# Performance work log

Hardware: AMD Instinct MI355X
Metric: run time of the kernel (lower is better)

Reference implementation:

```python
import jax, jax.numpy as jnp
import numpy as np

N = 50000; E = 120000; FN = 64; EA = 16; R = 4; H = 4; HID = 128; L = 3
NIDS = 10001; IDE = 32; RED = 8; NG = 64; NC = 10; KH = 128; GRID = 5; ORD = 3
EDIM = EA + RED; FFH = 256; GK = GRID + ORD


def layernorm(x, w, b):
    m = x.mean(-1, keepdims=True)
    v = ((x - m) ** 2).mean(-1, keepdims=True)
    return (x - m) / jnp.sqrt(v + 1e-5) * w + b


def b_splines(x, grid, k):
    # x: (B, in); grid: (in, G + 2k + 1) -> bases: (B, in, G + k)
    xe = x[..., None]
    bases = ((xe >= grid[:, :-1]) & (xe < grid[:, 1:])).astype(x.dtype)
    for j in range(1, k + 1):
        bases = ((xe - grid[:, :-(j + 1)]) / (grid[:, j:-1] - grid[:, :-(j + 1)]) * bases[..., :-1]
                 + (grid[:, j + 1:] - xe) / (grid[:, j + 1:] - grid[:, 1:-j]) * bases[..., 1:])
    return bases


def kan_linear(x, bw, sw, sc, grid):
    base = jax.nn.silu(x) @ bw.T
    B = b_splines(x, grid, ORD)
    return base + jnp.einsum('big,oig->bo', B, sw * sc[..., None])


def make_grid(in_features):
    h = 2.0 / GRID
    g = np.arange(-ORD, GRID + ORD + 1) * h - 1.0
    return jnp.asarray(np.tile(g, (in_features, 1)), dtype=jnp.float32)


def setup_inputs():
    key = jax.random.key(0)
    ks = jax.random.split(key, 24)
    s = 0.02
    inp = {}
    inp['x'] = jax.random.normal(ks[0], (N, FN), jnp.float32)
    inp['edge_attr'] = jax.random.normal(ks[1], (E, EA), jnp.float32)
    inp['id_token'] = jax.random.randint(ks[2], (N,), 0, NIDS)
    inp['edge_index'] = jax.random.randint(ks[3], (2, E), 0, N)
    inp['edge_type'] = jax.random.randint(ks[4], (E,), 0, R)
    inp['batch'] = jnp.sort(jax.random.randint(ks[5], (N,), 0, NG))
    inp['id_emb_table'] = jax.random.normal(ks[6], (NIDS, IDE)) * s
    inp['in_proj_w'] = jax.random.normal(ks[7], (HID, FN + IDE)) * s
    inp['in_proj_b'] = jnp.zeros((HID,))
    inp['rel_emb'] = jax.random.normal(ks[8], (L, R, RED)) * s
    inp['lin_l_w'] = jax.random.normal(ks[9], (L, R, H * HID, HID)) * s
    inp['lin_l_b'] = jnp.zeros((L, R, H * HID))
    inp['lin_r_w'] = jax.random.normal(ks[10], (L, R, H * HID, HID)) * s
    inp['lin_r_b'] = jnp.zeros((L, R, H * HID))
    inp['lin_edge_w'] = jax.random.normal(ks[11], (L, R, H * HID, EDIM)) * s
    inp['att_w'] = jax.random.normal(ks[12], (L, R, H, HID)) * s
    inp['conv_bias'] = jnp.zeros((L, R, HID))
    inp['rel_gate'] = jnp.zeros((L, R))
    inp['norm1_w'] = jnp.ones((L, HID)); inp['norm1_b'] = jnp.zeros((L, HID))
    inp['norm2_w'] = jnp.ones((L, HID)); inp['norm2_b'] = jnp.zeros((L, HID))
    inp['ffn_w1'] = jax.random.normal(ks[13], (L, FFH, HID)) * s
    inp['ffn_b1'] = jnp.zeros((L, FFH))
    inp['ffn_w2'] = jax.random.normal(ks[14], (L, HID, FFH)) * s
    inp['ffn_b2'] = jnp.zeros((L, HID))
    inp['readout_norm_w'] = jnp.ones((2 * HID,)); inp['readout_norm_b'] = jnp.zeros((2 * HID,))
    inp['base_w1'] = jax.random.normal(ks[15], (KH, 2 * HID)) * s
    inp['spline_w1'] = jax.random.normal(ks[16], (KH, 2 * HID, GK)) * s
    inp['spline_scaler1'] = jnp.ones((KH, 2 * HID))
    inp['grid1'] = make_grid(2 * HID)
    inp['base_w2'] = jax.random.normal(ks[17], (NC, KH)) * s
    inp['spline_w2'] = jax.random.normal(ks[18], (NC, KH, GK)) * s
    inp['spline_scaler2'] = jnp.ones((NC, KH))
    inp['grid2'] = make_grid(KH)
    return inp


def reference(x, edge_attr, id_token, edge_index, edge_type, batch,
              id_emb_table, in_proj_w, in_proj_b, rel_emb,
              lin_l_w, lin_l_b, lin_r_w, lin_r_b, lin_edge_w, att_w, conv_bias,
              rel_gate, norm1_w, norm1_b, norm2_w, norm2_b,
              ffn_w1, ffn_b1, ffn_w2, ffn_b2, readout_norm_w, readout_norm_b,
              base_w1, spline_w1, spline_scaler1, grid1,
              base_w2, spline_w2, spline_scaler2, grid2):
    src, dst = edge_index[0], edge_index[1]
    h = jnp.concatenate([x, id_emb_table[id_token]], -1)
    h = jax.nn.silu(h @ in_proj_w.T + in_proj_b)  # input_proj (eval: no dropout)
    for l in range(L):
        gate = jax.nn.softmax(rel_gate[l])  # all relations present w.h.p.
        h_msg = jnp.zeros_like(h)
        for r in range(R):
            maskf = (edge_type == r).astype(h.dtype)
            ea = jnp.concatenate([edge_attr, jnp.broadcast_to(rel_emb[l, r], (E, RED))], -1)
            xl = (h @ lin_l_w[l, r].T + lin_l_b[l, r]).reshape(N, H, HID)
            xr = (h @ lin_r_w[l, r].T + lin_r_b[l, r]).reshape(N, H, HID)
            ee = (ea @ lin_edge_w[l, r].T).reshape(E, H, HID)
            sfeat = jax.nn.leaky_relu(xl[src] + xr[dst] + ee, negative_slope=0.2)
            logit = jnp.einsum('ehc,hc->eh', sfeat, att_w[l, r])
            logit = jnp.where(maskf[:, None] > 0, logit, -1e9)
            m = jax.ops.segment_max(logit, dst, num_segments=N)
            a = jnp.exp(logit - m[dst]) * maskf[:, None]
            den = jax.ops.segment_sum(a, dst, num_segments=N)
            a = a / jnp.where(den == 0, 1.0, den)[dst]
            out = jax.ops.segment_sum(a[:, :, None] * xl[src], dst, num_segments=N)
            out = out.mean(1) + conv_bias[l, r]  # concat=False -> head mean
            h_msg = h_msg + gate[r] * out
        h = layernorm(h + h_msg, norm1_w[l], norm1_b[l])
        f = jax.nn.silu(h @ ffn_w1[l].T + ffn_b1[l]) @ ffn_w2[l].T + ffn_b2[l]
        h = layernorm(h + f, norm2_w[l], norm2_b[l])
    cnt = jax.ops.segment_sum(jnp.ones((N,), h.dtype), batch, num_segments=NG)
    hmean = jax.ops.segment_sum(h, batch, num_segments=NG) / jnp.maximum(cnt, 1.0)[:, None]
    hmax = jax.ops.segment_max(h, batch, num_segments=NG)
    g = layernorm(jnp.concatenate([hmean, hmax], -1), readout_norm_w, readout_norm_b)
    z = kan_linear(g, base_w1, spline_w1, spline_scaler1, grid1)
    logits = kan_linear(z, base_w2, spline_w2, spline_scaler2, grid2)
    return logits
```

## Files before the change

kernel.cpp:

```cpp
#include <hip/hip_runtime.h>
#include <math.h>

#define NN 50000
#define NE 120000
#define FN 64
#define NEA 16
#define NR 4
#define NH 4
#define HID 128
#define NL 3
#define IDE 32
#define RED 8
#define NG 64
#define NC 10
#define KH 128
#define FFH 256
#define NBIN (NR * NN)
#define SCAN_BLK ((NBIN + 1023) / 1024)
#define CAPS 32768
#define CAPH 9216

typedef short bf16x8 __attribute__((ext_vector_type(8)));
typedef float f32x4 __attribute__((ext_vector_type(4)));

__device__ __forceinline__ unsigned short f2b(float f) {
  unsigned u = __float_as_uint(f);
  unsigned r = (u + 0x7FFFu + ((u >> 16) & 1u)) >> 16;
  return (unsigned short)r;
}
__device__ __forceinline__ float b2f(unsigned short b) {
  return __uint_as_float((unsigned)b << 16);
}

__global__ void cvt_bf16(const float* __restrict__ s, unsigned short* __restrict__ d, int n4) {
  int i = blockIdx.x * blockDim.x + threadIdx.x;
  if (i >= n4) return;
  float4 v = ((const float4*)s)[i];
  ushort4 o;
  o.x = f2b(v.x); o.y = f2b(v.y); o.z = f2b(v.z); o.w = f2b(v.w);
  ((ushort4*)d)[i] = o;
}

template <int KT>
__device__ __forceinline__ void gemm_direct(
    const unsigned short* __restrict__ A, const int* __restrict__ rowlist,
    const unsigned short* __restrict__ W, const float* __restrict__ bias,
    float* __restrict__ Cf, unsigned short* __restrict__ Cb,
    int nrows, int mout, int act, int rowBase, int colBase) {
  constexpr int NK = KT / 32;
  __shared__ unsigned short Es[64][136];
  int t = threadIdx.x;
  int lane = t & 63, w = t >> 6;
  int wm = w >> 1, wn = w & 1;
  int q = lane >> 4, mr = lane & 15;

  const unsigned short* ap[2];
#pragma unroll
  for (int mt = 0; mt < 2; ++mt) {
    int gr = rowBase + wm * 32 + mt * 16 + mr;
    int cg = (gr < nrows) ? gr : 0;
    int ar = rowlist ? rowlist[cg] : cg;
    ap[mt] = A + (size_t)ar * KT + q * 8;
  }
  const unsigned short* wp[4];
#pragma unroll
  for (int nt = 0; nt < 4; ++nt)
    wp[nt] = W + (size_t)(colBase + wn * 64 + nt * 16 + mr) * KT + q * 8;

  f32x4 acc[2][4] = {};
#pragma unroll
  for (int k = 0; k < NK; ++k) {
    bf16x8 af[2], bfr[4];
#pragma unroll
    for (int mt = 0; mt < 2; ++mt) af[mt] = *(const bf16x8*)(ap[mt] + k * 32);
#pragma unroll
    for (int nt = 0; nt < 4; ++nt) bfr[nt] = *(const bf16x8*)(wp[nt] + k * 32);
#pragma unroll
    for (int mt = 0; mt < 2; ++mt)
#pragma unroll
      for (int nt = 0; nt < 4; ++nt)
        acc[mt][nt] = __builtin_amdgcn_mfma_f32_16x16x32_bf16(af[mt], bfr[nt], acc[mt][nt], 0, 0, 0);
  }

  float bv[4];
#pragma unroll
  for (int nt = 0; nt < 4; ++nt) bv[nt] = bias[colBase + wn * 64 + nt * 16 + mr];

  if (Cf) {
#pragma unroll
    for (int mt = 0; mt < 2; ++mt)
#pragma unroll
      for (int nt = 0; nt < 4; ++nt)
#pragma unroll
        for (int r = 0; r < 4; ++r) {
          int row = rowBase + wm * 32 + mt * 16 + q * 4 + r;
          int col = colBase + wn * 64 + nt * 16 + mr;
          if (row < nrows) {
            float v = acc[mt][nt][r] + bv[nt];
            if (act) v = v / (1.f + expf(-v));
            Cf[(size_t)row * mout + col] = v;
            if (Cb) Cb[(size_t)row * mout + col] = f2b(v);
          }
        }
  } else {
#pragma unroll
    for (int mt = 0; mt < 2; ++mt)
#pragma unroll
      for (int nt = 0; nt < 4; ++nt)
#pragma unroll
        for (int r = 0; r < 4; ++r) {
          float v = acc[mt][nt][r] + bv[nt];
          if (act) v = v / (1.f + expf(-v));
          Es[wm * 32 + mt * 16 + q * 4 + r][wn * 64 + nt * 16 + mr] = f2b(v);
        }
    __syncthreads();
    int rl = t >> 2, co = (t & 3) * 32;
    int grow = rowBase + rl;
    if (grow < nrows) {
      unsigned short* dst = Cb + (size_t)grow * mout + colBase + co;
#pragma unroll
      for (int j = 0; j < 4; ++j)
        *(bf16x8*)(dst + j * 8) = *(const bf16x8*)&Es[rl][co + j * 8];
    }
  }
}

template <int KT>
__global__ __launch_bounds__(256, 2) void gemm_bf16_t(
    const unsigned short* __restrict__ A, const unsigned short* __restrict__ W,
    const float* __restrict__ bias, float* __restrict__ Cf, unsigned short* __restrict__ Cb,
    int nrows, int mout, int act, int ncol) {
  int nbr = (nrows + 63) >> 6;
  int rpx = (nbr + 7) >> 3;
  int xcd = blockIdx.x & 7, j = blockIdx.x >> 3;
  int rowT = xcd * rpx + j / ncol;
  int cy = j - (j / ncol) * ncol;
  if (rowT >= nbr) return;
  gemm_direct<KT>(A, nullptr, W, bias, Cf, Cb, nrows, mout, act, rowT * 64, cy * 128);
}

__global__ __launch_bounds__(256, 2) void conv_xl_all(
    const unsigned short* __restrict__ hbf,
    const int* __restrict__ srclist, const int* __restrict__ hotlist,
    const int* __restrict__ cnts,
    const unsigned short* __restrict__ Wl, const float* __restrict__ bl,
    const unsigned short* __restrict__ Wr, const float* __restrict__ br,
    unsigned short* __restrict__ xlb, unsigned short* __restrict__ xrh) {
  for (int tid = blockIdx.x;; tid += gridDim.x) {
    int rem = tid, seg = 0, nrows = 0;
    for (; seg < 8; ++seg) {
      int r = seg >> 1;
      int n = (seg & 1) ? cnts[64 + r * 16] : cnts[128 + r * 16];
      int cap = (seg & 1) ? CAPH : CAPS;
      if (n > cap) n = cap;
      int tseg = ((n + 63) >> 6) * 4;
      if (rem < tseg) { nrows = n; break; }
      rem -= tseg;
    }
    if (seg == 8) return;
    int r = seg >> 1, sel = seg & 1;
    int rt = rem >> 2, ct = rem & 3;
    const int* list = (sel ? hotlist : srclist) + r * NN;
    const unsigned short* W = (sel ? Wr : Wl) + (size_t)r * 512 * 128;
    const float* bias = (sel ? br : bl) + (size_t)r * 512;
    unsigned short* C = sel ? (xrh + (size_t)r * CAPH * 512) : (xlb + (size_t)r * CAPS * 512);
    gemm_direct<128>(hbf, list, W, bias, nullptr, C, nrows, 512, 0, rt * 64, ct * 128);
    __syncthreads();
  }
}

__global__ __launch_bounds__(256, 2) void solo_gemm(
    const unsigned short* __restrict__ hbf,
    const int* __restrict__ solosrc, const int* __restrict__ solodst,
    const int* __restrict__ nsolo,
    const unsigned short* __restrict__ wsum, const float* __restrict__ bsum,
    const float* __restrict__ gate, float* __restrict__ hmsg) {
  int t = threadIdx.x, lane = t & 63, w = t >> 6;
  int wm = w >> 1, wn = w & 1, q = lane >> 4, mr = lane & 15;
  for (int tid = blockIdx.x;; tid += gridDim.x) {
    int rem = tid, r = 0, n = 0;
    for (; r < NR; ++r) {
      n = nsolo[r * 16];
      int ts = (n + 63) >> 6;
      if (rem < ts) break;
      rem -= ts;
    }
    if (r == NR) return;
    int rowBase = rem * 64;
    const unsigned short* ap[2];
#pragma unroll
    for (int mt = 0; mt < 2; ++mt) {
      int gr = rowBase + wm * 32 + mt * 16 + mr;
      int idx = (gr < n) ? solosrc[r * NN + gr] : 0;
      ap[mt] = hbf + (size_t)idx * HID + q * 8;
    }
    const unsigned short* wp[4];
#pragma unroll
    for (int nt = 0; nt < 4; ++nt)
      wp[nt] = wsum + (size_t)r * 16384 + (size_t)(wn * 64 + nt * 16 + mr) * HID + q * 8;
    f32x4 acc[2][4] = {};
#pragma unroll
    for (int k = 0; k < 4; ++k) {
      bf16x8 af[2], bfr[4];
#pragma unroll
      for (int mt = 0; mt < 2; ++mt) af[mt] = *(const bf16x8*)(ap[mt] + k * 32);
#pragma unroll
      for (int nt = 0; nt < 4; ++nt) bfr[nt] = *(const bf16x8*)(wp[nt] + k * 32);
#pragma unroll
      for (int mt = 0; mt < 2; ++mt)
#pragma unroll
        for (int nt = 0; nt < 4; ++nt)
          acc[mt][nt] = __builtin_amdgcn_mfma_f32_16x16x32_bf16(af[mt], bfr[nt], acc[mt][nt], 0, 0, 0);
    }
    float g4 = gate[r] * 0.25f;
    float bv[4];
#pragma unroll
    for (int nt = 0; nt < 4; ++nt) bv[nt] = bsum[r * 128 + wn * 64 + nt * 16 + mr];
#pragma unroll
    for (int mt = 0; mt < 2; ++mt)
#pragma unroll
      for (int rr = 0; rr < 4; ++rr) {
        int row = rowBase + wm * 32 + mt * 16 + q * 4 + rr;
        if (row < n) {
          int dst = solodst[r * NN + row];
#pragma unroll
          for (int nt = 0; nt < 4; ++nt) {
            int col = wn * 64 + nt * 16 + mr;
            atomicAdd(&hmsg[(size_t)dst * HID + col], g4 * (acc[mt][nt][rr] + bv[nt]));
          }
        }
      }
  }
}

__global__ void wsum_build(const float* __restrict__ linlw, const float* __restrict__ linlb,
                           unsigned short* __restrict__ wsum, float* __restrict__ bsum) {
  int i = blockIdx.x * blockDim.x + threadIdx.x;
  if (i >= NL * NR * 128 * 128) return;
  int k = i & 127, o = (i >> 7) & 127, lr = i >> 14;
  float s = 0.f;
#pragma unroll
  for (int h = 0; h < NH; ++h) s += linlw[((size_t)lr * 512 + h * 128 + o) * 128 + k];
  wsum[i] = f2b(s);
  if (k == 0) {
    float b = 0.f;
#pragma unroll
    for (int h = 0; h < NH; ++h) b += linlb[(size_t)lr * 512 + h * 128 + o];
    bsum[lr * 128 + o] = b;
  }
}

__global__ __launch_bounds__(256, 2) void layer_tail(
    float* __restrict__ h, const float* __restrict__ hmsg, const float* __restrict__ cb,
    const float* __restrict__ n1w, const float* __restrict__ n1b,
    const unsigned short* __restrict__ W1, const float* __restrict__ b1,
    const unsigned short* __restrict__ W2, const float* __restrict__ b2,
    const float* __restrict__ n2w, const float* __restrict__ n2b,
    unsigned short* __restrict__ hbfout) {
  __shared__ __align__(16) char smem[64 * 136 * 2 + 64 * 264 * 2];
  unsigned short (*Y)[136] = (unsigned short (*)[136])smem;
  unsigned short (*F1)[264] = (unsigned short (*)[264])(smem + 64 * 136 * 2);
  float (*Ef)[132] = (float (*)[132])(smem + 64 * 136 * 2);
  int nbr = (NN + 63) >> 6;
  int rpx = (nbr + 7) >> 3;
  int xcd = blockIdx.x & 7, j = blockIdx.x >> 3;
  int rowT = xcd * rpx + j;
  if (rowT >= nbr) return;
  int rowBase = rowT * 64;

  int t = threadIdx.x;
  int lane = t & 63, w = t >> 6;
  int wm = w >> 1, wn = w & 1;
  int q = lane >> 4, mr = lane & 15;

  {
    float w0 = n1w[lane], w1 = n1w[64 + lane];
    float bb0 = n1b[lane], bb1 = n1b[64 + lane];
    float c0 = cb[lane], c1 = cb[64 + lane];
    for (int rr = w; rr < 64; rr += 4) {
      int grow = rowBase + rr;
      if (grow < NN) {
        size_t base = (size_t)grow * HID;
        float x0 = h[base + lane] + hmsg[base + lane] + c0;
        float x1 = h[base + 64 + lane] + hmsg[base + 64 + lane] + c1;
        float s = x0 + x1;
#pragma unroll
        for (int o = 32; o > 0; o >>= 1) s += __shfl_xor(s, o, 64);
        float mean = s * (1.f / 128.f);
        float d0 = x0 - mean, d1 = x1 - mean;
        float v = d0 * d0 + d1 * d1;
#pragma unroll
        for (int o = 32; o > 0; o >>= 1) v += __shfl_xor(v, o, 64);
        float inv = 1.f / sqrtf(v * (1.f / 128.f) + 1e-5f);
        float y0 = d0 * inv * w0 + bb0;
        float y1 = d1 * inv * w1 + bb1;
        h[base + lane] = y0;
        h[base + 64 + lane] = y1;
        Y[rr][lane] = f2b(y0);
        Y[rr][64 + lane] = f2b(y1);
      } else {
        Y[rr][lane] = 0;
        Y[rr][64 + lane] = 0;
      }
    }
  }
  __syncthreads();

  bf16x8 a[2][4];
#pragma unroll
  for (int mt = 0; mt < 2; ++mt)
#pragma unroll
    for (int k = 0; k < 4; ++k)
      a[mt][k] = *(const bf16x8*)&Y[wm * 32 + mt * 16 + mr][k * 32 + q * 8];

#pragma unroll
  for (int ph = 0; ph < 2; ++ph) {
    const unsigned short* wp[4];
#pragma unroll
    for (int nt = 0; nt < 4; ++nt)
      wp[nt] = W1 + (size_t)(ph * 128 + wn * 64 + nt * 16 + mr) * HID + q * 8;
    f32x4 acc[2][4] = {};
#pragma unroll
    for (int k = 0; k < 4; ++k) {
      bf16x8 bfr[4];
#pragma unroll
      for (int nt = 0; nt < 4; ++nt) bfr[nt] = *(const bf16x8*)(wp[nt] + k * 32);
#pragma unroll
      for (int mt = 0; mt < 2; ++mt)
#pragma unroll
        for (int nt = 0; nt < 4; ++nt)
          acc[mt][nt] = __builtin_amdgcn_mfma_f32_16x16x32_bf16(a[mt][k], bfr[nt], acc[mt][nt], 0, 0, 0);
    }
    float bv[4];
#pragma unroll
    for (int nt = 0; nt < 4; ++nt) bv[nt] = b1[ph * 128 + wn * 64 + nt * 16 + mr];
#pragma unroll
    for (int mt = 0; mt < 2; ++mt)
#pragma unroll
      for (int nt = 0; nt < 4; ++nt)
#pragma unroll
        for (int r = 0; r < 4; ++r) {
          float v = acc[mt][nt][r] + bv[nt];
          v = v / (1.f + expf(-v));
          F1[wm * 32 + mt * 16 + q * 4 + r][ph * 128 + wn * 64 + nt * 16 + mr] = f2b(v);
        }
  }
  __syncthreads();

  const unsigned short* wp2[4];
#pragma unroll
  for (int nt = 0; nt < 4; ++nt)
    wp2[nt] = W2 + (size_t)(wn * 64 + nt * 16 + mr) * FFH + q * 8;
  f32x4 acc2[2][4] = {};
#pragma unroll
  for (int k = 0; k < 8; ++k) {
    bf16x8 af[2], bfr[4];
#pragma unroll
    for (int mt = 0; mt < 2; ++mt)
      af[mt] = *(const bf16x8*)&F1[wm * 32 + mt * 16 + mr][k * 32 + q * 8];
#pragma unroll
    for (int nt = 0; nt < 4; ++nt) bfr[nt] = *(const bf16x8*)(wp2[nt] + k * 32);
#pragma unroll
    for (int mt = 0; mt < 2; ++mt)
#pragma unroll
      for (int nt = 0; nt < 4; ++nt)
        acc2[mt][nt] = __builtin_amdgcn_mfma_f32_16x16x32_bf16(af[mt], bfr[nt], acc2[mt][nt], 0, 0, 0);
  }
  __syncthreads();

  float bv2[4];
#pragma unroll
  for (int nt = 0; nt < 4; ++nt) bv2[nt] = b2[wn * 64 + nt * 16 + mr];
#pragma unroll
  for (int mt = 0; mt < 2; ++mt)
#pragma unroll
    for (int nt = 0; nt < 4; ++nt)
#pragma unroll
      for (int r = 0; r < 4; ++r)
        Ef[wm * 32 + mt * 16 + q * 4 + r][wn * 64 + nt * 16 + mr] = acc2[mt][nt][r] + bv2[nt];
  __syncthreads();

  float w0 = n2w[lane], w1 = n2w[64 + lane];
  float bb0 = n2b[lane], bb1 = n2b[64 + lane];
  for (int rr = w; rr < 64; rr += 4) {
    int grow = rowBase + rr;
    if (grow >= NN) continue;
    size_t base = (size_t)grow * HID;
    float x0 = h[base + lane] + Ef[rr][lane];
    float x1 = h[base + 64 + lane] + Ef[rr][64 + lane];
    float s = x0 + x1;
#pragma unroll
    for (int o = 32; o > 0; o >>= 1) s += __shfl_xor(s, o, 64);
    float mean = s * (1.f / 128.f);
    float d0 = x0 - mean, d1 = x1 - mean;
    float v = d0 * d0 + d1 * d1;
#pragma unroll
    for (int o = 32; o > 0; o >>= 1) v += __shfl_xor(v, o, 64);
    float inv = 1.f / sqrtf(v * (1.f / 128.f) + 1e-5f);
    float y0 = d0 * inv * w0 + bb0;
    float y1 = d1 * inv * w1 + bb1;
    h[base + lane] = y0;
    h[base + 64 + lane] = y1;
    hbfout[base + lane] = f2b(y0);
    hbfout[base + 64 + lane] = f2b(y1);
  }
}

__global__ void build_xin_bf(const float* __restrict__ x, const int* __restrict__ idtok,
                             const float* __restrict__ emb, unsigned short* __restrict__ xin) {
  int i = blockIdx.x * blockDim.x + threadIdx.x;
  if (i >= NN * 96) return;
  int n = i / 96, k = i - n * 96;
  float v = (k < FN) ? x[(size_t)n * FN + k] : emb[(size_t)idtok[n] * IDE + (k - FN)];
  xin[i] = f2b(v);
}

__global__ void hist_bin(const int* __restrict__ ei, const int* __restrict__ et,
                         int* __restrict__ bcnt) {
  int e = blockIdx.x * blockDim.x + threadIdx.x;
  if (e >= NE) return;
  atomicAdd(&bcnt[et[e] * NN + ei[NE + e]], 1);
}
__global__ __launch_bounds__(256) void scan1(const int* __restrict__ cnt,
                                             int* __restrict__ pos, int* __restrict__ bsum) {
  __shared__ int lds[256];
  int b = blockIdx.x, t = threadIdx.x;
  int base = b * 1024 + t * 4;
  int v[4];
#pragma unroll
  for (int j = 0; j < 4; ++j) v[j] = (base + j < NBIN) ? cnt[base + j] : 0;
  int tot = v[0] + v[1] + v[2] + v[3];
  lds[t] = tot;
  __syncthreads();
  for (int off = 1; off < 256; off <<= 1) {
    int x = (t >= off) ? lds[t - off] : 0;
    __syncthreads();
    lds[t] += x;
    __syncthreads();
  }
  if (t == 255) bsum[b] = lds[255];
  int run = lds[t] - tot;
#pragma unroll
  for (int j = 0; j < 4; ++j) {
    if (base + j < NBIN) pos[base + j] = run;
    run += v[j];
  }
}
__global__ __launch_bounds__(256) void scan2(int* __restrict__ bsum) {
  __shared__ int lds[256];
  int t = threadIdx.x;
  int v = (t < SCAN_BLK) ? bsum[t] : 0;
  lds[t] = v;
  __syncthreads();
  for (int off = 1; off < 256; off <<= 1) {
    int x = (t >= off) ? lds[t - off] : 0;
    __syncthreads();
    lds[t] += x;
    __syncthreads();
  }
  if (t < SCAN_BLK) bsum[t] = lds[t] - v;
}
__global__ void scan3(int* __restrict__ pos, const int* __restrict__ bsum,
                      const int* __restrict__ cnt) {
  int i = blockIdx.x * blockDim.x + threadIdx.x;
  if (i >= NBIN) return;
  pos[i] += bsum[i >> 10];
  if (i == NBIN - 1) pos[NBIN] = pos[i] + cnt[i];
}
__global__ void scatter_bin(const int* __restrict__ ei, const int* __restrict__ et,
                            const int* __restrict__ csroff, int* __restrict__ cur,
                            int* __restrict__ elist) {
  int e = blockIdx.x * blockDim.x + threadIdx.x;
  if (e >= NE) return;
  int bin = et[e] * NN + ei[NE + e];
  int p = atomicAdd(&cur[bin], 1);
  elist[csroff[bin] + p] = e;
}
__global__ void sort_bins(const int* __restrict__ csroff, int* __restrict__ elist) {
  int b = blockIdx.x * blockDim.x + threadIdx.x;
  if (b >= NBIN) return;
  int s = csroff[b], e = csroff[b + 1];
  for (int i = s + 1; i < e; ++i) {
    int key = elist[i];
    int j = i - 1;
    while (j >= s && elist[j] > key) { elist[j + 1] = elist[j]; --j; }
    elist[j + 1] = key;
  }
}
__global__ void gather_edge(const int* __restrict__ ei, const int* __restrict__ elist,
                            const float* __restrict__ eattr,
                            int* __restrict__ rsrc, float* __restrict__ eacsr) {
  int p = blockIdx.x * blockDim.x + threadIdx.x;
  if (p >= NE) return;
  int e = elist[p];
  rsrc[p] = ei[e];
  const float4* s = (const float4*)(eattr + (size_t)e * NEA);
  float4* d = (float4*)(eacsr + (size_t)p * NEA);
#pragma unroll
  for (int j = 0; j < 4; ++j) d[j] = s[j];
}
__global__ void mark_hotsrc(const int* __restrict__ csroff, const int* __restrict__ rsrc,
                            int* __restrict__ srcflag) {
  int b = blockIdx.x * blockDim.x + threadIdx.x;
  if (b >= NBIN) return;
  int s = csroff[b], e = csroff[b + 1];
  if (e - s < 2) return;
  int rel = b / NN;
  for (int p = s; p < e; ++p) srcflag[rel * NN + rsrc[p]] = 1;
}
__global__ void build_src_o(const int* __restrict__ srcflag, const int* __restrict__ srcpos,
                            int* __restrict__ srclist, int* __restrict__ srcmap) {
  int b = blockIdx.x * blockDim.x + threadIdx.x;
  if (b >= NBIN) return;
  if (srcflag[b]) {
    int rel = b / NN;
    int pos = srcpos[b] - srcpos[rel * NN];
    srcmap[b] = pos;
    srclist[rel * NN + pos] = b - rel * NN;
  }
}
__global__ void fincnt(const int* __restrict__ srcpos, int* __restrict__ nsrc) {
  int r = threadIdx.x;
  if (r < NR) nsrc[r * 16] = srcpos[(r + 1) * NN] - srcpos[r * NN];
}
__global__ void remap_rsrc(const int* __restrict__ csroff, const int* __restrict__ rsrc,
                           const int* __restrict__ srcmap, int* __restrict__ rsrcx) {
  int p = blockIdx.x * blockDim.x + threadIdx.x;
  if (p >= NE) return;
  int rel = (p >= csroff[NN]) + (p >= csroff[2 * NN]) + (p >= csroff[3 * NN]);
  rsrcx[p] = srcmap[rel * NN + rsrc[p]];
}
__global__ __launch_bounds__(256) void build_hot(
    const int* __restrict__ csroff, const int* __restrict__ rsrc,
    int* __restrict__ nsolo, int* __restrict__ nhot,
    int* __restrict__ solosrc, int* __restrict__ solodst, int* __restrict__ hotlist) {
  __shared__ int wsc[4][4], whc[4][4];
  __shared__ int sbase[4], hbase[4];
  int t = threadIdx.x, wave = t >> 6, lane = t & 63;
  int b = blockIdx.x * 256 + t;
  bool valid = b < NBIN;
  int cnt = 0, rel = 0, s = 0;
  if (valid) { s = csroff[b]; cnt = csroff[b + 1] - s; rel = b / NN; }
  bool solo = valid && cnt == 1;
  bool hot = valid && cnt >= 2;
#pragma unroll
  for (int rr = 0; rr < 4; ++rr) {
    unsigned long long ms = __ballot(solo && rel == rr);
    unsigned long long mh = __ballot(hot && rel == rr);
    if (lane == 0) { wsc[wave][rr] = __popcll(ms); whc[wave][rr] = __popcll(mh); }
  }
  __syncthreads();
  if (t < 4) {
    int ssum = wsc[0][t] + wsc[1][t] + wsc[2][t] + wsc[3][t];
    int hsum = whc[0][t] + whc[1][t] + whc[2][t] + whc[3][t];
    sbase[t] = ssum ? atomicAdd(&nsolo[t * 16], ssum) : 0;
    hbase[t] = hsum ? atomicAdd(&nhot[t * 16], hsum) : 0;
  }
  __syncthreads();
#pragma unroll
  for (int rr = 0; rr < 4; ++rr) {
    unsigned long long ms = __ballot(solo && rel == rr);
    if (solo && rel == rr) {
      int before = 0;
#pragma unroll
      for (int wv = 0; wv < 4; ++wv) if (wv < wave) before += wsc[wv][rr];
      int pos = sbase[rr] + before + __popcll(ms & ((1ull << lane) - 1ull));
      solosrc[rr * NN + pos] = rsrc[s];
      solodst[rr * NN + pos] = b - rr * NN;
    }
    unsigned long long mh = __ballot(hot && rel == rr);
    if (hot && rel == rr) {
      int before = 0;
#pragma unroll
      for (int wv = 0; wv < 4; ++wv) if (wv < wave) before += whc[wv][rr];
      int pos = hbase[rr] + before + __popcll(mh & ((1ull << lane) - 1ull));
      hotlist[rr * NN + pos] = b - rr * NN;
    }
  }
}

__global__ void gate_cb_all(const float* __restrict__ rg, const float* __restrict__ cbias,
                            float* __restrict__ gate, float* __restrict__ cb) {
  __shared__ float g[NR];
  int l = blockIdx.x, t = threadIdx.x;
  const float* rgl = rg + l * NR;
  if (t == 0) {
    float mx = rgl[0];
    for (int r = 1; r < NR; ++r) mx = fmaxf(mx, rgl[r]);
    float s = 0.f, tmp[NR];
    for (int r = 0; r < NR; ++r) { tmp[r] = expf(rgl[r] - mx); s += tmp[r]; }
    for (int r = 0; r < NR; ++r) { g[r] = tmp[r] / s; gate[l * NR + r] = g[r]; }
  }
  __syncthreads();
  float c = 0.f;
  for (int r = 0; r < NR; ++r) c += g[r] * cbias[(size_t)l * NR * HID + r * HID + t];
  cb[l * HID + t] = c;
}

__global__ __launch_bounds__(256) void edge_all(
    const int* __restrict__ csroff, const int* __restrict__ rsrcx,
    const float* __restrict__ eacsr, const float* __restrict__ relembp,
    const float* __restrict__ wedgep, const float* __restrict__ attwp,
    const unsigned short* __restrict__ xlb, const unsigned short* __restrict__ xrh,
    const int* __restrict__ hotlist, const int* __restrict__ nhot,
    float* __restrict__ hmsg, const float* __restrict__ gate, int rel) {
  __shared__ float lds[4][128];
  int wave = threadIdx.x >> 6, lane = threadIdx.x & 63;
  float g4 = gate[rel] * 0.25f;
  int hh = wave;
  float wreg[2][24], areg[2];
#pragma unroll
  for (int j = 0; j < 2; ++j) {
    int col = hh * 128 + j * 64 + lane;
    const float* wp = wedgep + (size_t)col * 24;
#pragma unroll
    for (int k = 0; k < 24; ++k) wreg[j][k] = wp[k];
    areg[j] = attwp[col];
  }
  float evr0 = 0.f, evr1 = 0.f;
#pragma unroll
  for (int k = 0; k < 8; ++k) {
    float rk = relembp[k];
    evr0 += rk * wreg[0][NEA + k];
    evr1 += rk * wreg[1][NEA + k];
  }
  int nh = nhot[rel * 16];
  for (int wi = blockIdx.x; wi < nh; wi += gridDim.x) {
    int dst = hotlist[rel * NN + wi];
    int s = csroff[rel * NN + dst], e = csroff[rel * NN + dst + 1];
    {
      const unsigned short* xrp = xrh + (size_t)wi * 512;
      float xr0 = b2f(xrp[hh * 128 + lane]);
      float xr1 = b2f(xrp[hh * 128 + 64 + lane]);
      float m = -3.4e38f, den = 0.f, acc0 = 0.f, acc1 = 0.f;
      for (int p = s; p < e; ++p) {
        int src = rsrcx[p];
        const float* eap = eacsr + (size_t)p * NEA;
        float eev0 = evr0, eev1 = evr1;
#pragma unroll
        for (int k = 0; k < NEA; ++k) {
          float er = eap[k];
          eev0 += er * wreg[0][k];
          eev1 += er * wreg[1][k];
        }
        float xl0 = b2f(xlb[(size_t)src * 512 + hh * 128 + lane]);
        float xl1 = b2f(xlb[(size_t)src * 512 + hh * 128 + 64 + lane]);
        float s0 = xl0 + xr0 + eev0; s0 = (s0 > 0.f) ? s0 : 0.2f * s0;
        float s1 = xl1 + xr1 + eev1; s1 = (s1 > 0.f) ? s1 : 0.2f * s1;
        float lg = s0 * areg[0] + s1 * areg[1];
#pragma unroll
        for (int o = 32; o > 0; o >>= 1) lg += __shfl_xor(lg, o, 64);
        float mn = fmaxf(m, lg);
        float sc = expf(m - mn);
        float ex = expf(lg - mn);
        den = den * sc + ex;
        acc0 = acc0 * sc + ex * xl0;
        acc1 = acc1 * sc + ex * xl1;
        m = mn;
      }
      float wgt = g4 / den;
      lds[wave][lane] = acc0 * wgt;
      lds[wave][64 + lane] = acc1 * wgt;
    }
    __syncthreads();
    if (wave < 2) {
      int d = wave * 64 + lane;
      float v = lds[0][d] + lds[1][d] + lds[2][d] + lds[3][d];
      hmsg[(size_t)dst * HID + d] += v;
    }
    __syncthreads();
  }
}

__global__ void group_bounds(const int* __restrict__ batch, int* __restrict__ gstart) {
  int g = threadIdx.x + blockIdx.x * blockDim.x;
  if (g > NG) return;
  int lo = 0, hi = NN;
  while (lo < hi) {
    int mid = (lo + hi) >> 1;
    if (batch[mid] < g) lo = mid + 1; else hi = mid;
  }
  gstart[g] = lo;
}
__global__ __launch_bounds__(128) void readout_part2(
    const float* __restrict__ h, const int* __restrict__ gstart,
    float* __restrict__ psum, float* __restrict__ pmax) {
  int g = blockIdx.x, s = blockIdx.y, t = threadIdx.x;
  int r0 = gstart[g], r1 = gstart[g + 1];
  float acc = 0.f, mx = -3.4e38f;
  for (int row = r0 + s; row < r1; row += 8) {
    float v = h[(size_t)row * HID + t];
    acc += v;
    mx = fmaxf(mx, v);
  }
  psum[((size_t)g * 8 + s) * HID + t] = acc;
  pmax[((size_t)g * 8 + s) * HID + t] = mx;
}
__global__ __launch_bounds__(256) void readout_final(
    const int* __restrict__ gstart, const float* __restrict__ psum,
    const float* __restrict__ pmax, const float* __restrict__ w,
    const float* __restrict__ b, float* __restrict__ g) {
  int bg = blockIdx.x, t = threadIdx.x;
  __shared__ float red[256];
  float c = fmaxf((float)(gstart[bg + 1] - gstart[bg]), 1.f);
  float x;
  if (t < HID) {
    float ssum = 0.f;
    for (int s = 0; s < 8; ++s) ssum += psum[((size_t)bg * 8 + s) * HID + t];
    x = ssum / c;
  } else {
    float mx = -3.4e38f;
    for (int s = 0; s < 8; ++s) mx = fmaxf(mx, pmax[((size_t)bg * 8 + s) * HID + (t - HID)]);
    x = mx;
  }
  red[t] = x;
  __syncthreads();
  for (int s = 128; s > 0; s >>= 1) {
    if (t < s) red[t] += red[t + s];
    __syncthreads();
  }
  float mean = red[0] * (1.f / 256.f);
  __syncthreads();
  float d = x - mean;
  red[t] = d * d;
  __syncthreads();
  for (int s = 128; s > 0; s >>= 1) {
    if (t < s) red[t] += red[t + s];
    __syncthreads();
  }
  float inv = 1.f / sqrtf(red[0] * (1.f / 256.f) + 1e-5f);
  g[(size_t)bg * 256 + t] = d * inv * w[t] + b[t];
}

__device__ __forceinline__ void bspline8(float x, const float* __restrict__ t,
                                         float* __restrict__ out) {
  float bs[11];
#pragma unroll
  for (int j = 0; j < 11; ++j) bs[j] = (x >= t[j] && x < t[j + 1]) ? 1.f : 0.f;
#pragma unroll
  for (int k = 1; k <= 3; ++k) {
    for (int j = 0; j < 11 - k; ++j) {
      bs[j] = (x - t[j]) / (t[j + k] - t[j]) * bs[j] +
              (t[j + k + 1] - x) / (t[j + k + 1] - t[j + 1]) * bs[j + 1];
    }
  }
#pragma unroll
  for (int j = 0; j < 8; ++j) out[j] = bs[j];
}

__global__ __launch_bounds__(128) void kan1_part(
    const float* __restrict__ g, const float* __restrict__ bw,
    const float* __restrict__ sw, const float* __restrict__ sc,
    const float* __restrict__ grid, float* __restrict__ zpart) {
  int bg = blockIdx.x, ch = blockIdx.y, t = threadIdx.x;
  int base = ch * 32;
  __shared__ float B[32][8];
  __shared__ float sg[32];
  if (t < 32) {
    float x = g[(size_t)bg * 256 + base + t];
    sg[t] = x / (1.f + expf(-x));
    bspline8(x, grid + (size_t)(base + t) * 12, B[t]);
  }
  __syncthreads();
  float acc = 0.f;
  for (int i = 0; i < 32; ++i) {
    int col = base + i;
    acc += sg[i] * bw[(size_t)t * 256 + col];
    const float* swp = sw + ((size_t)t * 256 + col) * 8;
    float sp = 0.f;
#pragma unroll
    for (int k = 0; k < 8; ++k) sp += B[i][k] * swp[k];
    acc += sp * sc[(size_t)t * 256 + col];
  }
  zpart[((size_t)ch * NG + bg) * KH + t] = acc;
}

__global__ __launch_bounds__(128) void kan2(
    const float* __restrict__ zpart, const float* __restrict__ bw,
    const float* __restrict__ sw, const float* __restrict__ sc,
    const float* __restrict__ grid, float* __restrict__ out) {
  int bg = blockIdx.x, t = threadIdx.x;
  __shared__ float B[128][8];
  __shared__ float sz[128];
  float x = 0.f;
  for (int ch = 0; ch < 8; ++ch) x += zpart[((size_t)ch * NG + bg) * KH + t];
  sz[t] = x / (1.f + expf(-x));
  bspline8(x, grid + (size_t)t * 12, B[t]);
  __syncthreads();
  if (t < NC) {
    float acc = 0.f;
    for (int i = 0; i < 128; ++i) {
      acc += sz[i] * bw[(size_t)t * 128 + i];
      const float* swp = sw + ((size_t)t * 128 + i) * 8;
      float sp = 0.f;
#pragma unroll
      for (int k = 0; k < 8; ++k) sp += B[i][k] * swp[k];
      acc += sp * sc[(size_t)t * 128 + i];
    }
    out[(size_t)bg * NC + t] = acc;
  }
}

extern "C" void kernel_launch(void* const* d_in, const int* in_sizes, int n_in,
                              void* d_out, int out_size, void* d_ws, size_t ws_size,
                              hipStream_t stream) {
  const float* x       = (const float*)d_in[0];
  const float* eattr   = (const float*)d_in[1];
  const int*   idtok   = (const int*)d_in[2];
  const int*   ei      = (const int*)d_in[3];
  const int*   etype   = (const int*)d_in[4];
  const int*   batch   = (const int*)d_in[5];
  const float* idemb   = (const float*)d_in[6];
  const float* inw     = (const float*)d_in[7];
  const float* inb     = (const float*)d_in[8];
  const float* relemb  = (const float*)d_in[9];
  const float* linlw   = (const float*)d_in[10];
  const float* linlb   = (const float*)d_in[11];
  const float* linrw   = (const float*)d_in[12];
  const float* linrb   = (const float*)d_in[13];
  const float* linew   = (const float*)d_in[14];
  const float* attw    = (const float*)d_in[15];
  const float* convb   = (const float*)d_in[16];
  const float* relgate = (const float*)d_in[17];
  const float* n1w     = (const float*)d_in[18];
  const float* n1b     = (const float*)d_in[19];
  const float* n2w     = (const float*)d_in[20];
  const float* n2b     = (const float*)d_in[21];
  const float* f1w     = (const float*)d_in[22];
  const float* f1bias  = (const float*)d_in[23];
  const float* f2w     = (const float*)d_in[24];
  const float* f2bias  = (const float*)d_in[25];
  const float* rnw     = (const float*)d_in[26];
  const float* rnb     = (const float*)d_in[27];
  const float* bw1     = (const float*)d_in[28];
  const float* sw1     = (const float*)d_in[29];
  const float* sc1     = (const float*)d_in[30];
  const float* grid1   = (const float*)d_in[31];
  const float* bw2     = (const float*)d_in[32];
  const float* sw2     = (const float*)d_in[33];
  const float* sc2     = (const float*)d_in[34];
  const float* grid2   = (const float*)d_in[35];
  float* out = (float*)d_out;
  (void)in_sizes; (void)n_in; (void)out_size; (void)ws_size;

  char* p = (char*)d_ws;
  auto alloc = [&](size_t bytes) { void* q = (void*)p; p += (bytes + 255) & ~(size_t)255; return q; };
  float* h    = (float*)alloc((size_t)NN * HID * 4);
  float* hmsg = (float*)alloc((size_t)NN * HID * 4);
  unsigned short* hbf = (unsigned short*)alloc((size_t)NN * HID * 2);
  unsigned short* xlb = (unsigned short*)alloc((size_t)NR * CAPS * 512 * 2);
  unsigned short* xrh = (unsigned short*)alloc((size_t)NR * CAPH * 512 * 2);
  int* elist = (int*)alloc((size_t)NE * 4);
  int* rsrc  = (int*)alloc((size_t)NE * 4);
  int* rsrcx = (int*)alloc((size_t)NE * 4);
  float* eacsr = (float*)alloc((size_t)NE * NEA * 4);
  int* bcnt  = (int*)alloc((size_t)NBIN * 8 + 8);
  int* cur   = bcnt + NBIN;
  int* csroff = (int*)alloc((size_t)(NBIN + 1) * 4);
  int* srcpos = (int*)alloc((size_t)(NBIN + 1) * 4);
  int* bsum  = (int*)alloc((size_t)SCAN_BLK * 4);
  int* hotlist = (int*)alloc((size_t)NR * NN * 4);
  int* solosrc = (int*)alloc((size_t)NR * NN * 4);
  int* solodst = (int*)alloc((size_t)NR * NN * 4);
  int* srclist = (int*)alloc((size_t)NR * NN * 4);
  int* srcflag = (int*)alloc((size_t)NBIN * 4);
  int* srcmap  = (int*)alloc((size_t)NBIN * 4);
  int* cnts    = (int*)alloc(1024);
  int* nsolo   = cnts;
  int* nhot    = cnts + 64;
  int* nsrc    = cnts + 128;
  unsigned short* linlwb = (unsigned short*)alloc((size_t)NL * NR * 512 * 128 * 2);
  unsigned short* linrwb = (unsigned short*)alloc((size_t)NL * NR * 512 * 128 * 2);
  unsigned short* f1wb   = (unsigned short*)alloc((size_t)NL * 256 * 128 * 2);
  unsigned short* f2wb   = (unsigned short*)alloc((size_t)NL * 128 * 256 * 2);
  unsigned short* inwb   = (unsigned short*)alloc((size_t)128 * 96 * 2);
  unsigned short* wsumb  = (unsigned short*)alloc((size_t)NL * NR * 128 * 128 * 2);
  float* bsumf = (float*)alloc((size_t)NL * NR * 128 * 4);
  float* gate = (float*)alloc(NL * NR * 4);
  float* cb   = (float*)alloc(NL * HID * 4);
  int* gstart = (int*)alloc((size_t)(NG + 1) * 4);
  float* psum = (float*)alloc((size_t)NG * 8 * HID * 4);
  float* pmax = (float*)alloc((size_t)NG * 8 * HID * 4);
  float* zpart = (float*)alloc((size_t)8 * NG * KH * 4);
  float* g = (float*)alloc((size_t)NG * 256 * 4);
  unsigned short* xinbf = xlb;

  const int NB64 = (NN + 63) / 64;
  const int RPX = (NB64 + 7) / 8;

  {
    int n;
    n = NL * NR * 512 * 128 / 4;
    cvt_bf16<<<(n + 255) / 256, 256, 0, stream>>>(linlw, linlwb, n);
    cvt_bf16<<<(n + 255) / 256, 256, 0, stream>>>(linrw, linrwb, n);
    n = NL * 256 * 128 / 4;
    cvt_bf16<<<(n + 255) / 256, 256, 0, stream>>>(f1w, f1wb, n);
    cvt_bf16<<<(n + 255) / 256, 256, 0, stream>>>(f2w, f2wb, n);
    n = 128 * 96 / 4;
    cvt_bf16<<<(n + 255) / 256, 256, 0, stream>>>(inw, inwb, n);
  }
  wsum_build<<<(NL * NR * 128 * 128 + 255) / 256, 256, 0, stream>>>(linlw, linlb, wsumb, bsumf);

  hipMemsetAsync(bcnt, 0, (size_t)NBIN * 8 + 8, stream);
  hipMemsetAsync(srcflag, 0, (size_t)NBIN * 4, stream);
  hipMemsetAsync(cnts, 0, 1024, stream);
  hist_bin<<<(NE + 255) / 256, 256, 0, stream>>>(ei, etype, bcnt);
  scan1<<<SCAN_BLK, 256, 0, stream>>>(bcnt, csroff, bsum);
  scan2<<<1, 256, 0, stream>>>(bsum);
  scan3<<<(NBIN + 255) / 256, 256, 0, stream>>>(csroff, bsum, bcnt);
  scatter_bin<<<(NE + 255) / 256, 256, 0, stream>>>(ei, etype, csroff, cur, elist);
  sort_bins<<<(NBIN + 255) / 256, 256, 0, stream>>>(csroff, elist);
  gather_edge<<<(NE + 255) / 256, 256, 0, stream>>>(ei, elist, eattr, rsrc, eacsr);
  mark_hotsrc<<<(NBIN + 255) / 256, 256, 0, stream>>>(csroff, rsrc, srcflag);
  scan1<<<SCAN_BLK, 256, 0, stream>>>(srcflag, srcpos, bsum);
  scan2<<<1, 256, 0, stream>>>(bsum);
  scan3<<<(NBIN + 255) / 256, 256, 0, stream>>>(srcpos, bsum, srcflag);
  build_src_o<<<(NBIN + 255) / 256, 256, 0, stream>>>(srcflag, srcpos, srclist, srcmap);
  fincnt<<<1, 64, 0, stream>>>(srcpos, nsrc);
  remap_rsrc<<<(NE + 255) / 256, 256, 0, stream>>>(csroff, rsrc, srcmap, rsrcx);
  build_hot<<<(NBIN + 255) / 256, 256, 0, stream>>>(csroff, rsrc, nsolo, nhot,
                                                    solosrc, solodst, hotlist);
  gate_cb_all<<<NL, 128, 0, stream>>>(relgate, convb, gate, cb);

  build_xin_bf<<<(NN * 96 + 255) / 256, 256, 0, stream>>>(x, idtok, idemb, xinbf);
  gemm_bf16_t<96><<<8 * RPX, 256, 0, stream>>>(xinbf, inwb, inb, h, hbf, NN, 128, 1, 1);

  for (int l = 0; l < NL; ++l) {
    hipMemsetAsync(hmsg, 0, (size_t)NN * HID * 4, stream);
    solo_gemm<<<2048, 256, 0, stream>>>(
        hbf, solosrc, solodst, nsolo,
        wsumb + (size_t)l * NR * 16384, bsumf + (size_t)l * NR * 128,
        gate + l * NR, hmsg);
    conv_xl_all<<<4096, 256, 0, stream>>>(
        hbf, srclist, hotlist, cnts,
        linlwb + (size_t)l * NR * 512 * 128, linlb + (size_t)l * NR * 512,
        linrwb + (size_t)l * NR * 512 * 128, linrb + (size_t)l * NR * 512,
        xlb, xrh);
    for (int r = 0; r < NR; ++r) {
      int lr = l * NR + r;
      edge_all<<<4096, 256, 0, stream>>>(
          csroff, rsrcx, eacsr, relemb + (size_t)lr * RED,
          linew + (size_t)lr * 512 * 24,
          attw + (size_t)lr * 512,
          xlb + (size_t)r * CAPS * 512, xrh + (size_t)r * CAPH * 512,
          hotlist, nhot, hmsg, gate + l * NR, r);
    }
    layer_tail<<<8 * RPX, 256, 0, stream>>>(
        h, hmsg, cb + l * HID, n1w + l * HID, n1b + l * HID,
        f1wb + (size_t)l * 256 * 128, f1bias + (size_t)l * 256,
        f2wb + (size_t)l * 128 * 256, f2bias + (size_t)l * 128,
        n2w + l * HID, n2b + l * HID, hbf);
  }

  group_bounds<<<1, 128, 0, stream>>>(batch, gstart);
  readout_part2<<<dim3(NG, 8), 128, 0, stream>>>(h, gstart, psum, pmax);
  readout_final<<<NG, 256, 0, stream>>>(gstart, psum, pmax, rnw, rnb, g);
  kan1_part<<<dim3(NG, 8), 128, 0, stream>>>(g, bw1, sw1, sc1, grid1, zpart);
  kan2<<<NG, 128, 0, stream>>>(zpart, bw2, sw2, sc2, grid2, out);
}
```

Before: 1.156 ms.

## Fuse solo GEMM into conv projection kernel and zero hmsg inside layer tail

```diff
diff --git a/kernel.cpp b/kernel.cpp
--- a/kernel.cpp
+++ b/kernel.cpp
@@ -139,97 +139,92 @@
   gemm_direct<KT>(A, nullptr, W, bias, Cf, Cb, nrows, mout, act, rowT * 64, cy * 128);
 }
 
-__global__ __launch_bounds__(256, 2) void conv_xl_all(
+__global__ __launch_bounds__(256, 2) void conv_solo_all(
     const unsigned short* __restrict__ hbf,
     const int* __restrict__ srclist, const int* __restrict__ hotlist,
     const int* __restrict__ cnts,
     const unsigned short* __restrict__ Wl, const float* __restrict__ bl,
     const unsigned short* __restrict__ Wr, const float* __restrict__ br,
-    unsigned short* __restrict__ xlb, unsigned short* __restrict__ xrh) {
-  for (int tid = blockIdx.x;; tid += gridDim.x) {
-    int rem = tid, seg = 0, nrows = 0;
-    for (; seg < 8; ++seg) {
-      int r = seg >> 1;
-      int n = (seg & 1) ? cnts[64 + r * 16] : cnts[128 + r * 16];
-      int cap = (seg & 1) ? CAPH : CAPS;
-      if (n > cap) n = cap;
-      int tseg = ((n + 63) >> 6) * 4;
-      if (rem < tseg) { nrows = n; break; }
-      rem -= tseg;
-    }
-    if (seg == 8) return;
-    int r = seg >> 1, sel = seg & 1;
-    int rt = rem >> 2, ct = rem & 3;
-    const int* list = (sel ? hotlist : srclist) + r * NN;
-    const unsigned short* W = (sel ? Wr : Wl) + (size_t)r * 512 * 128;
-    const float* bias = (sel ? br : bl) + (size_t)r * 512;
-    unsigned short* C = sel ? (xrh + (size_t)r * CAPH * 512) : (xlb + (size_t)r * CAPS * 512);
-    gemm_direct<128>(hbf, list, W, bias, nullptr, C, nrows, 512, 0, rt * 64, ct * 128);
-    __syncthreads();
-  }
-}
-
-__global__ __launch_bounds__(256, 2) void solo_gemm(
-    const unsigned short* __restrict__ hbf,
+    unsigned short* __restrict__ xlb, unsigned short* __restrict__ xrh,
     const int* __restrict__ solosrc, const int* __restrict__ solodst,
-    const int* __restrict__ nsolo,
     const unsigned short* __restrict__ wsum, const float* __restrict__ bsum,
     const float* __restrict__ gate, float* __restrict__ hmsg) {
   int t = threadIdx.x, lane = t & 63, w = t >> 6;
   int wm = w >> 1, wn = w & 1, q = lane >> 4, mr = lane & 15;
   for (int tid = blockIdx.x;; tid += gridDim.x) {
-    int rem = tid, r = 0, n = 0;
-    for (; r < NR; ++r) {
-      n = nsolo[r * 16];
-      int ts = (n + 63) >> 6;
-      if (rem < ts) break;
-      rem -= ts;
-    }
-    if (r == NR) return;
-    int rowBase = rem * 64;
-    const unsigned short* ap[2];
-#pragma unroll
-    for (int mt = 0; mt < 2; ++mt) {
-      int gr = rowBase + wm * 32 + mt * 16 + mr;
-      int idx = (gr < n) ? solosrc[r * NN + gr] : 0;
-      ap[mt] = hbf + (size_t)idx * HID + q * 8;
-    }
-    const unsigned short* wp[4];
-#pragma unroll
-    for (int nt = 0; nt < 4; ++nt)
-      wp[nt] = wsum + (size_t)r * 16384 + (size_t)(wn * 64 + nt * 16 + mr) * HID + q * 8;
-    f32x4 acc[2][4] = {};
-#pragma unroll
-    for (int k = 0; k < 4; ++k) {
-      bf16x8 af[2], bfr[4];
-#pragma unroll
-      for (int mt = 0; mt < 2; ++mt) af[mt] = *(const bf16x8*)(ap[mt] + k * 32);
-#pragma unroll
-      for (int nt = 0; nt < 4; ++nt) bfr[nt] = *(const bf16x8*)(wp[nt] + k * 32);
+    int rem = tid, seg = 0, nrows = 0;
+    for (; seg < 12; ++seg) {
+      int n, tseg;
+      if (seg < 8) {
+        int r = seg >> 1;
+        n = (seg & 1) ? cnts[64 + r * 16] : cnts[128 + r * 16];
+        int cap = (seg & 1) ? CAPH : CAPS;
+        if (n > cap) n = cap;
+        tseg = ((n + 63) >> 6) * 4;
+      } else {
+        n = cnts[(seg - 8) * 16];
+        tseg = (n + 63) >> 6;
+      }
+      if (rem < tseg) { nrows = n; break; }
+      rem -= tseg;
+    }
+    if (seg == 12) return;
+    if (seg < 8) {
+      int r = seg >> 1, sel = seg & 1;
+      int rt = rem >> 2, ct = rem & 3;
+      const int* list = (sel ? hotlist : srclist) + r * NN;
+      const unsigned short* W = (sel ? Wr : Wl) + (size_t)r * 512 * 128;
+      const float* bias = (sel ? br : bl) + (size_t)r * 512;
+      unsigned short* C = sel ? (xrh + (size_t)r * CAPH * 512) : (xlb + (size_t)r * CAPS * 512);
+      gemm_direct<128>(hbf, list, W, bias, nullptr, C, nrows, 512, 0, rt * 64, ct * 128);
+    } else {
+      int r = seg - 8;
+      int rowBase = rem * 64;
+      const unsigned short* ap[2];
+#pragma unroll
+      for (int mt = 0; mt < 2; ++mt) {
+        int gr = rowBase + wm * 32 + mt * 16 + mr;
+        int idx = (gr < nrows) ? solosrc[r * NN + gr] : 0;
+        ap[mt] = hbf + (size_t)idx * HID + q * 8;
+      }
+      const unsigned short* wp[4];
+#pragma unroll
+      for (int nt = 0; nt < 4; ++nt)
+        wp[nt] = wsum + (size_t)r * 16384 + (size_t)(wn * 64 + nt * 16 + mr) * HID + q * 8;
+      f32x4 acc[2][4] = {};
+#pragma unroll
+      for (int k = 0; k < 4; ++k) {
+        bf16x8 af[2], bfr[4];
+#pragma unroll
+        for (int mt = 0; mt < 2; ++mt) af[mt] = *(const bf16x8*)(ap[mt] + k * 32);
+#pragma unroll
+        for (int nt = 0; nt < 4; ++nt) bfr[nt] = *(const bf16x8*)(wp[nt] + k * 32);
+#pragma unroll
+        for (int mt = 0; mt < 2; ++mt)
+#pragma unroll
+          for (int nt = 0; nt < 4; ++nt)
+            acc[mt][nt] = __builtin_amdgcn_mfma_f32_16x16x32_bf16(af[mt], bfr[nt], acc[mt][nt], 0, 0, 0);
+      }
+      float g4 = gate[r] * 0.25f;
+      float bv[4];
+#pragma unroll
+      for (int nt = 0; nt < 4; ++nt) bv[nt] = bsum[r * 128 + wn * 64 + nt * 16 + mr];
 #pragma unroll
       for (int mt = 0; mt < 2; ++mt)
 #pragma unroll
-        for (int nt = 0; nt < 4; ++nt)
-          acc[mt][nt] = __builtin_amdgcn_mfma_f32_16x16x32_bf16(af[mt], bfr[nt], acc[mt][nt], 0, 0, 0);
-    }
-    float g4 = gate[r] * 0.25f;
-    float bv[4];
-#pragma unroll
-    for (int nt = 0; nt < 4; ++nt) bv[nt] = bsum[r * 128 + wn * 64 + nt * 16 + mr];
-#pragma unroll
-    for (int mt = 0; mt < 2; ++mt)
-#pragma unroll
-      for (int rr = 0; rr < 4; ++rr) {
-        int row = rowBase + wm * 32 + mt * 16 + q * 4 + rr;
-        if (row < n) {
-          int dst = solodst[r * NN + row];
-#pragma unroll
-          for (int nt = 0; nt < 4; ++nt) {
-            int col = wn * 64 + nt * 16 + mr;
-            atomicAdd(&hmsg[(size_t)dst * HID + col], g4 * (acc[mt][nt][rr] + bv[nt]));
+        for (int rr = 0; rr < 4; ++rr) {
+          int row = rowBase + wm * 32 + mt * 16 + q * 4 + rr;
+          if (row < nrows) {
+            int dst = solodst[r * NN + row];
+#pragma unroll
+            for (int nt = 0; nt < 4; ++nt) {
+              int col = wn * 64 + nt * 16 + mr;
+              atomicAdd(&hmsg[(size_t)dst * HID + col], g4 * (acc[mt][nt][rr] + bv[nt]));
+            }
           }
         }
-      }
+    }
+    __syncthreads();
   }
 }
 
@@ -251,7 +246,7 @@
 }
 
 __global__ __launch_bounds__(256, 2) void layer_tail(
-    float* __restrict__ h, const float* __restrict__ hmsg, const float* __restrict__ cb,
+    float* __restrict__ h, float* __restrict__ hmsg, const float* __restrict__ cb,
     const float* __restrict__ n1w, const float* __restrict__ n1b,
     const unsigned short* __restrict__ W1, const float* __restrict__ b1,
     const unsigned short* __restrict__ W2, const float* __restrict__ b2,
@@ -273,16 +268,21 @@
   int wm = w >> 1, wn = w & 1;
   int q = lane >> 4, mr = lane & 15;
 
+  float y0r[16], y1r[16];
   {
     float w0 = n1w[lane], w1 = n1w[64 + lane];
     float bb0 = n1b[lane], bb1 = n1b[64 + lane];
     float c0 = cb[lane], c1 = cb[64 + lane];
-    for (int rr = w; rr < 64; rr += 4) {
+#pragma unroll
+    for (int it = 0; it < 16; ++it) {
+      int rr = it * 4 + w;
       int grow = rowBase + rr;
       if (grow < NN) {
         size_t base = (size_t)grow * HID;
         float x0 = h[base + lane] + hmsg[base + lane] + c0;
         float x1 = h[base + 64 + lane] + hmsg[base + 64 + lane] + c1;
+        hmsg[base + lane] = 0.f;
+        hmsg[base + 64 + lane] = 0.f;
         float s = x0 + x1;
 #pragma unroll
         for (int o = 32; o > 0; o >>= 1) s += __shfl_xor(s, o, 64);
@@ -294,11 +294,13 @@
         float inv = 1.f / sqrtf(v * (1.f / 128.f) + 1e-5f);
         float y0 = d0 * inv * w0 + bb0;
         float y1 = d1 * inv * w1 + bb1;
-        h[base + lane] = y0;
-        h[base + 64 + lane] = y1;
+        y0r[it] = y0;
+        y1r[it] = y1;
         Y[rr][lane] = f2b(y0);
         Y[rr][64 + lane] = f2b(y1);
       } else {
+        y0r[it] = 0.f;
+        y1r[it] = 0.f;
         Y[rr][lane] = 0;
         Y[rr][64 + lane] = 0;
       }
@@ -382,12 +384,14 @@
 
   float w0 = n2w[lane], w1 = n2w[64 + lane];
   float bb0 = n2b[lane], bb1 = n2b[64 + lane];
-  for (int rr = w; rr < 64; rr += 4) {
+#pragma unroll
+  for (int it = 0; it < 16; ++it) {
+    int rr = it * 4 + w;
     int grow = rowBase + rr;
     if (grow >= NN) continue;
     size_t base = (size_t)grow * HID;
-    float x0 = h[base + lane] + Ef[rr][lane];
-    float x1 = h[base + 64 + lane] + Ef[rr][64 + lane];
+    float x0 = y0r[it] + Ef[rr][lane];
+    float x1 = y1r[it] + Ef[rr][64 + lane];
     float s = x0 + x1;
 #pragma unroll
     for (int o = 32; o > 0; o >>= 1) s += __shfl_xor(s, o, 64);
@@ -925,17 +929,16 @@
   build_xin_bf<<<(NN * 96 + 255) / 256, 256, 0, stream>>>(x, idtok, idemb, xinbf);
   gemm_bf16_t<96><<<8 * RPX, 256, 0, stream>>>(xinbf, inwb, inb, h, hbf, NN, 128, 1, 1);
 
+  hipMemsetAsync(hmsg, 0, (size_t)NN * HID * 4, stream);
   for (int l = 0; l < NL; ++l) {
-    hipMemsetAsync(hmsg, 0, (size_t)NN * HID * 4, stream);
-    solo_gemm<<<2048, 256, 0, stream>>>(
-        hbf, solosrc, solodst, nsolo,
-        wsumb + (size_t)l * NR * 16384, bsumf + (size_t)l * NR * 128,
-        gate + l * NR, hmsg);
-    conv_xl_all<<<4096, 256, 0, stream>>>(
+    conv_solo_all<<<4096, 256, 0, stream>>>(
         hbf, srclist, hotlist, cnts,
         linlwb + (size_t)l * NR * 512 * 128, linlb + (size_t)l * NR * 512,
         linrwb + (size_t)l * NR * 512 * 128, linrb + (size_t)l * NR * 512,
-        xlb, xrh);
+        xlb, xrh,
+        solosrc, solodst,
+        wsumb + (size_t)l * NR * 16384, bsumf + (size_t)l * NR * 128,
+        gate + l * NR, hmsg);
     for (int r = 0; r < NR; ++r) {
       int lr = l * NR + r;
       edge_all<<<4096, 256, 0, stream>>>(
```

After: 1.060 ms. 8.4% less time.
